# Performance work log

Hardware: AMD Instinct MI355X
Metric: run time of the kernel (lower is better)

Reference implementation:

```python
import jax, jax.numpy as jnp
import numpy as np

B, N, NONGT, D, H, PE = 128, 36, 36, 1024, 16, 64
DG = D // H  # per-head dim = 64


def setup_inputs() -> dict:
    key = jax.random.key(0)
    ks = jax.random.split(key, 10)
    s = 0.02
    return {
        "roi_feat": jax.random.normal(ks[0], (B, N, D), jnp.float32),
        "adj_matrix": jax.random.randint(ks[1], (B, N, NONGT), 0, 2, jnp.int32),
        "position_embedding": jax.random.normal(ks[2], (B, N, NONGT, PE), jnp.float32),
        "label_biases_att": jax.random.normal(ks[3], (B, N, NONGT), jnp.float32) * 0.1,
        # effective (weight-normed) linear weights
        "Wq": jax.random.normal(ks[4], (D, D), jnp.float32) * s,
        "bq": jnp.zeros((D,), jnp.float32),
        "Wk": jax.random.normal(ks[5], (D, D), jnp.float32) * s,
        "bk": jnp.zeros((D,), jnp.float32),
        "Wpos": jax.random.normal(ks[6], (H, PE), jnp.float32) * s,
        "bpos": jnp.zeros((H,), jnp.float32),
        # grouped 1x1 conv (groups=H): per-head projection feat_dim -> feat_dim/H
        "Wout": jax.random.normal(ks[7], (H, DG, D), jnp.float32) * s,
        "bout": jnp.zeros((D,), jnp.float32),
    }


def reference(roi_feat, adj_matrix, position_embedding, label_biases_att,
              Wq, bq, Wk, bk, Wpos, bpos, Wout, bout):
    b, n, d = roi_feat.shape
    nongt = adj_matrix.shape[2]
    dg = d // H
    v = roi_feat[:, :nongt, :]                                  # [B,nongt,D]
    q = (roi_feat @ Wq.T + bq).reshape(b, n, H, dg)             # [B,N,H,dg]
    k = (v @ Wk.T + bk).reshape(b, nongt, H, dg)                # [B,nongt,H,dg]
    # scaled QK^T, laid out [B,N,H,nongt] (orig: matmul then transpose(1,2))
    aff = jnp.einsum('bnhd,bmhd->bnhm', q, k) / jnp.sqrt(jnp.float32(dg))
    # position log-bias
    pos = jax.nn.relu(position_embedding.reshape(b, n * nongt, -1) @ Wpos.T + bpos)
    pos = pos.reshape(b, n, nongt, H).transpose(0, 1, 3, 2)     # [B,N,H,nongt]
    waff = aff + jnp.log(jnp.maximum(pos, jnp.float32(1e-6)))
    # adjacency mask + label bias (orig does this in [B,N,nongt,H] layout; equivalent)
    mask = adj_matrix[:, :, None, :] > 0                        # [B,N,1,nongt]
    waff = jnp.where(mask, waff, jnp.float32(-9e15)) + label_biases_att[:, :, None, :]
    att = jax.nn.softmax(waff, axis=-1)                         # [B,N,H,nongt]
    # weighted sum of full V (note: V is full feat_dim per head, not dg)
    out_t = jnp.einsum('bnhm,bmd->bnhd', att, v)                # [B,N,H,D]
    # grouped 1x1 conv: per-head D -> D/H, heads concatenated
    out = jnp.einsum('bnhd,hed->bnhe', out_t, Wout).reshape(b, n, d) + bout
    return out
```

## Files before the change

kernel.cpp:

```cpp
#include <hip/hip_runtime.h>
#include <hip/hip_bf16.h>

#define BB 128
#define NN 36
#define DD 1024
#define HH 16
#define ROWS (BB*NN)

typedef __attribute__((ext_vector_type(8))) __bf16 bf16x8;
typedef __attribute__((ext_vector_type(4))) float f32x4;
typedef __attribute__((ext_vector_type(4))) unsigned short us4;

__device__ inline unsigned short f2bf(float f) {
    __hip_bfloat16 h = __float2bfloat16(f);
    return *reinterpret_cast<unsigned short*>(&h);
}

__device__ inline void async16(const unsigned short* g, unsigned short* l) {
    __builtin_amdgcn_global_load_lds((const __attribute__((address_space(1))) unsigned int*)g,
                                     (__attribute__((address_space(3))) unsigned int*)l, 16, 0, 0);
}

__global__ __launch_bounds__(256) void prep_kernel(const float* __restrict__ roi,
                                                   const float* __restrict__ Wq,
                                                   const float* __restrict__ Wk,
                                                   const float* __restrict__ Wout,
                                                   const float* __restrict__ pe,
                                                   const float* __restrict__ Wpos,
                                                   const float* __restrict__ bpos,
                                                   const int* __restrict__ adj,
                                                   const float* __restrict__ lbl,
                                                   unsigned short* __restrict__ roi_bf,
                                                   unsigned short* __restrict__ Wcat_bf,
                                                   float* __restrict__ extra) {
    const int bid = blockIdx.x, tid = threadIdx.x;
    if (bid < 4608) {
        int i = bid * 256 + tid;
        f32x4 v = ((const f32x4*)roi)[i];
        us4 o;
        o.x = f2bf(v[0]); o.y = f2bf(v[1]); o.z = f2bf(v[2]); o.w = f2bf(v[3]);
        ((us4*)roi_bf)[i] = o;
        return;
    }
    if (bid < 7680) {
        int wb = bid - 4608;
        int sel = wb >> 10;
        const float* src = sel == 0 ? Wq : (sel == 1 ? Wk : Wout);
        int i = (wb & 1023) * 256 + tid;
        f32x4 v = ((const f32x4*)src)[i];
        us4 o;
        o.x = f2bf(v[0]); o.y = f2bf(v[1]); o.z = f2bf(v[2]); o.w = f2bf(v[3]);
        ((us4*)(Wcat_bf + (size_t)sel * DD * DD))[i] = o;
        return;
    }
    __shared__ __align__(16) float wps[HH * 64];
    __shared__ float bps[HH];
    for (int i = tid; i < HH * 64; i += 256) wps[i] = Wpos[i];
    if (tid < HH) bps[tid] = bpos[tid];
    __syncthreads();

    int idx = (bid - 7680) * 256 + tid;
    f32x4 pr[16];
    const f32x4* pv = (const f32x4*)(pe + (size_t)idx * 64);
#pragma unroll
    for (int j = 0; j < 16; j++) pr[j] = pv[j];
    int a = adj[idx];
    float add = lbl[idx] + (a > 0 ? 0.f : -9e15f);
    int b = idx / 1296, nm = idx % 1296;
    size_t obase = (size_t)b * (16 * 1296) + nm;
    for (int hh = 0; hh < 16; hh++) {
        const f32x4* wv = (const f32x4*)(wps + hh * 64);
        f32x4 acc4 = {0.f, 0.f, 0.f, 0.f};
#pragma unroll
        for (int j = 0; j < 16; j++) acc4 += pr[j] * wv[j];
        float d = acc4[0] + acc4[1] + acc4[2] + acc4[3] + bps[hh];
        d = fmaxf(d, 0.f);
        d = __logf(fmaxf(d, 1e-6f));
        extra[obase + (size_t)hh * 1296] = d + add;
    }
}

__global__ __launch_bounds__(256, 2) void fused_kernel(const unsigned short* __restrict__ A,
                                                       const unsigned short* __restrict__ Wc,
                                                       const float* __restrict__ bq,
                                                       const float* __restrict__ bk,
                                                       const float* __restrict__ extra,
                                                       const float* __restrict__ bout,
                                                       float* __restrict__ out) {
    __shared__ __align__(16) unsigned short pool[21504];
    const int tid  = threadIdx.x;
    const int wave = tid >> 6, lane = tid & 63;
    const int quad = lane >> 4, l16 = lane & 15;
    const int h  = blockIdx.x & 15;
    const int bg = blockIdx.x >> 4;
    const int row0 = bg * 144;

    unsigned short* As = pool;
    unsigned short* Bs = pool + 9216;

    const unsigned short* gsrc[11];
    unsigned short* ldst[11];
#pragma unroll
    for (int i = 0; i < 11; i++) {
        int j = wave + 4 * i;
        int c = j * 64 + lane;
        if (j < 18) {
            int row = c >> 3;
            int col = ((c & 7) ^ (row & 7)) * 8;
            gsrc[i] = A + (size_t)(row0 + row) * DD + col;
            ldst[i] = As + j * 512;
        } else {
            int cb = c - 1152;
            int row = cb >> 3;
            int sec = row >> 6;
            int wrow = sec * DD + h * 64 + (row & 63);
            int col = ((cb & 7) ^ (row & 7)) * 8;
            gsrc[i] = Wc + (size_t)wrow * DD + col;
            ldst[i] = Bs + (j - 18) * 512;
        }
    }

    f32x4 acc[9][3] = {};

#pragma unroll
    for (int k0i = 0; k0i < 16; k0i++) {
#pragma unroll
        for (int i = 0; i < 11; i++) {
            if (i < 10 || wave < 2)
                async16(gsrc[i] + k0i * 64, ldst[i]);
        }
        __syncthreads();

#pragma unroll
        for (int ks = 0; ks < 2; ks++) {
            int kch = ks * 4 + quad;
            bf16x8 bfv[3], afv[9];
#pragma unroll
            for (int ct = 0; ct < 3; ct++) {
                int rowb = wave * 48 + ct * 16 + l16;
                bfv[ct] = *(const bf16x8*)&Bs[rowb * 64 + ((kch ^ (rowb & 7)) * 8)];
            }
#pragma unroll
            for (int rt = 0; rt < 9; rt++) {
                int rowa = rt * 16 + l16;
                afv[rt] = *(const bf16x8*)&As[rowa * 64 + ((kch ^ (rowa & 7)) * 8)];
            }
#pragma unroll
            for (int rt = 0; rt < 9; rt++)
#pragma unroll
                for (int ct = 0; ct < 3; ct++)
                    acc[rt][ct] = __builtin_amdgcn_mfma_f32_16x16x32_bf16(afv[rt], bfv[ct], acc[rt][ct], 0, 0, 0);
        }
        __syncthreads();
    }

    const int bat = wave;
    const float* exb = extra + ((size_t)((bg * 4 + bat) * 16 + h)) * 1296;
    float exv[3][4][3];
#pragma unroll
    for (int mt = 0; mt < 3; mt++)
#pragma unroll
        for (int r = 0; r < 4; r++) {
            int row = mt * 16 + quad * 4 + r;
#pragma unroll
            for (int nt = 0; nt < 3; nt++) {
                int col = nt * 16 + l16;
                exv[mt][r][nt] = (row < 36 && col < 36) ? exb[row * 36 + col] : 0.f;
            }
        }
    float bo[4];
#pragma unroll
    for (int nt = 0; nt < 4; nt++) bo[nt] = bout[h * 64 + nt * 16 + l16];

    unsigned short* qL = pool;
    unsigned short* kL = pool + 10368;
#pragma unroll
    for (int ct = 0; ct < 3; ct++) {
        int g = wave * 48 + ct * 16 + l16;
        int sec = g >> 6, e = g & 63;
        if (sec < 2) {
            unsigned short* dst = (sec == 0) ? qL : kL;
            float bias = (sec == 0) ? bq[h * 64 + e] : bk[h * 64 + e];
#pragma unroll
            for (int rt = 0; rt < 9; rt++)
#pragma unroll
                for (int r = 0; r < 4; r++) {
                    int row = rt * 16 + quad * 4 + r;
                    dst[row * 72 + e] = f2bf(acc[rt][ct][r] + bias);
                }
        }
    }
    __syncthreads();

    const unsigned short* qB = qL + bat * 36 * 72;
    const unsigned short* kB = kL + bat * 36 * 72;
    int rq[3];
#pragma unroll
    for (int t = 0; t < 3; t++) { int rr = t * 16 + l16; rq[t] = rr < 36 ? rr : 35; }

    f32x4 aff[3][3] = {};
#pragma unroll
    for (int ks = 0; ks < 2; ks++) {
        bf16x8 afr[3], bfr[3];
#pragma unroll
        for (int t = 0; t < 3; t++) afr[t] = *(const bf16x8*)&qB[rq[t] * 72 + ks * 32 + quad * 8];
#pragma unroll
        for (int t = 0; t < 3; t++) bfr[t] = *(const bf16x8*)&kB[rq[t] * 72 + ks * 32 + quad * 8];
#pragma unroll
        for (int mt = 0; mt < 3; mt++)
#pragma unroll
            for (int nt = 0; nt < 3; nt++)
                aff[mt][nt] = __builtin_amdgcn_mfma_f32_16x16x32_bf16(afr[mt], bfr[nt], aff[mt][nt], 0, 0, 0);
    }
    __syncthreads();

    unsigned short* vwT   = pool;
    unsigned short* attsL = pool + 10240 + bat * 2688;
#pragma unroll
    for (int mt = 0; mt < 3; mt++) {
#pragma unroll
        for (int r = 0; r < 4; r++) {
            int row = mt * 16 + quad * 4 + r;
            float w[3];
#pragma unroll
            for (int nt = 0; nt < 3; nt++) {
                int col = nt * 16 + l16;
                bool valid = (row < 36) && (col < 36);
                w[nt] = valid ? (aff[mt][nt][r] * 0.125f + exv[mt][r][nt]) : -3.4e38f;
            }
            float mx = fmaxf(fmaxf(w[0], w[1]), w[2]);
#pragma unroll
            for (int d = 1; d < 16; d <<= 1) mx = fmaxf(mx, __shfl_xor(mx, d));
            float e0 = __expf(w[0] - mx), e1 = __expf(w[1] - mx), e2 = __expf(w[2] - mx);
            float s = e0 + e1 + e2;
#pragma unroll
            for (int d = 1; d < 16; d <<= 1) s += __shfl_xor(s, d);
            float rs = 1.0f / s;
            attsL[row * 56 + 0  + l16] = f2bf(e0 * rs);
            attsL[row * 56 + 16 + l16] = f2bf(e1 * rs);
            attsL[row * 56 + 32 + l16] = f2bf(e2 * rs);
        }
    }
#pragma unroll
    for (int ct = 0; ct < 3; ct++) {
        int g = wave * 48 + ct * 16 + l16;
        int sec = g >> 6, e = g & 63;
        if (sec == 2) {
#pragma unroll
            for (int rt = 0; rt < 9; rt++)
#pragma unroll
                for (int r = 0; r < 4; r++) {
                    int row = rt * 16 + quad * 4 + r;
                    int bb = row / 36, m = row - bb * 36;
                    vwT[bb * 2560 + e * 40 + m] = f2bf(acc[rt][ct][r]);
                }
        }
    }
    __syncthreads();

    const unsigned short* vB = vwT + bat * 2560;
    f32x4 o[3][4] = {};
    {
        bf16x8 pa[3], pb[4], zf = {};
#pragma unroll
        for (int mt = 0; mt < 3; mt++) pa[mt] = *(const bf16x8*)&attsL[(mt * 16 + l16) * 56 + quad * 8];
#pragma unroll
        for (int nt = 0; nt < 4; nt++) pb[nt] = *(const bf16x8*)&vB[(nt * 16 + l16) * 40 + quad * 8];
#pragma unroll
        for (int mt = 0; mt < 3; mt++)
#pragma unroll
            for (int nt = 0; nt < 4; nt++)
                o[mt][nt] = __builtin_amdgcn_mfma_f32_16x16x32_bf16(pa[mt], pb[nt], o[mt][nt], 0, 0, 0);
#pragma unroll
        for (int mt = 0; mt < 3; mt++)
            pa[mt] = (quad < 2) ? *(const bf16x8*)&attsL[(mt * 16 + l16) * 56 + 32 + quad * 8] : zf;
#pragma unroll
        for (int nt = 0; nt < 4; nt++)
            pb[nt] = (quad < 2) ? *(const bf16x8*)&vB[(nt * 16 + l16) * 40 + 32 + quad * 8] : zf;
#pragma unroll
        for (int mt = 0; mt < 3; mt++)
#pragma unroll
            for (int nt = 0; nt < 4; nt++)
                o[mt][nt] = __builtin_amdgcn_mfma_f32_16x16x32_bf16(pa[mt], pb[nt], o[mt][nt], 0, 0, 0);
    }

    const size_t obase = (size_t)((bg * 4 + bat) * 36) * DD + h * 64;
#pragma unroll
    for (int mt = 0; mt < 3; mt++)
#pragma unroll
        for (int r = 0; r < 4; r++) {
            int n = mt * 16 + quad * 4 + r;
            if (n < 36) {
#pragma unroll
                for (int nt = 0; nt < 4; nt++)
                    out[obase + (size_t)n * DD + nt * 16 + l16] = o[mt][nt][r] + bo[nt];
            }
        }
}

extern "C" void kernel_launch(void* const* d_in, const int* in_sizes, int n_in,
                              void* d_out, int out_size, void* d_ws, size_t ws_size,
                              hipStream_t stream) {
    const float* roi  = (const float*)d_in[0];
    const int*   adj  = (const int*)  d_in[1];
    const float* pe   = (const float*)d_in[2];
    const float* lbl  = (const float*)d_in[3];
    const float* Wq   = (const float*)d_in[4];
    const float* bq   = (const float*)d_in[5];
    const float* Wk   = (const float*)d_in[6];
    const float* bk   = (const float*)d_in[7];
    const float* Wpos = (const float*)d_in[8];
    const float* bpos = (const float*)d_in[9];
    const float* Wout = (const float*)d_in[10];
    const float* bout = (const float*)d_in[11];
    float* out = (float*)d_out;

    char* w = (char*)d_ws;
    unsigned short* roi_bf  = (unsigned short*)(w);
    unsigned short* Wcat_bf = (unsigned short*)(w + 9437184);
    float*          extra   = (float*)(w + 15728640);

    prep_kernel<<<8328, 256, 0, stream>>>(roi, Wq, Wk, Wout, pe, Wpos, bpos, adj, lbl,
                                          roi_bf, Wcat_bf, extra);
    fused_kernel<<<32 * 16, 256, 0, stream>>>(roi_bf, Wcat_bf, bq, bk, extra, bout, out);
}
```

Baseline: 170.7 us.

## Replace async global-to-LDS loads with register-staged prefetch of next K tile

Switches the GEMM tile staging from direct global_load_lds intrinsics to loading the next K-slice into registers while the current slice is computed, then writing registers to LDS. This is meant to overlap global memory latency with MFMA work, where before each step waited on its own loads. It costs 11 extra vector registers per thread and an explicit LDS store pass, which could hurt occupancy under the 2-blocks launch bound. It also clamps an out-of-range B row index.

```diff
diff --git a/kernel.cpp b/kernel.cpp
--- a/kernel.cpp
+++ b/kernel.cpp
@@ -14,11 +14,6 @@
 __device__ inline unsigned short f2bf(float f) {
     __hip_bfloat16 h = __float2bfloat16(f);
     return *reinterpret_cast<unsigned short*>(&h);
-}
-
-__device__ inline void async16(const unsigned short* g, unsigned short* l) {
-    __builtin_amdgcn_global_load_lds((const __attribute__((address_space(1))) unsigned int*)g,
-                                     (__attribute__((address_space(3))) unsigned int*)l, 16, 0, 0);
 }
 
 __global__ __launch_bounds__(256) void prep_kernel(const float* __restrict__ roi,
@@ -98,8 +93,8 @@
     unsigned short* As = pool;
     unsigned short* Bs = pool + 9216;
 
-    const unsigned short* gsrc[11];
-    unsigned short* ldst[11];
+    const f32x4* gsrc[11];
+    f32x4* ldst[11];
 #pragma unroll
     for (int i = 0; i < 11; i++) {
         int j = wave + 4 * i;
@@ -107,29 +102,42 @@
         if (j < 18) {
             int row = c >> 3;
             int col = ((c & 7) ^ (row & 7)) * 8;
-            gsrc[i] = A + (size_t)(row0 + row) * DD + col;
-            ldst[i] = As + j * 512;
+            gsrc[i] = (const f32x4*)(A + (size_t)(row0 + row) * DD + col);
+            ldst[i] = (f32x4*)(As + j * 512 + lane * 8);
         } else {
             int cb = c - 1152;
             int row = cb >> 3;
+            if (row > 191) row = 191;
             int sec = row >> 6;
             int wrow = sec * DD + h * 64 + (row & 63);
             int col = ((cb & 7) ^ (row & 7)) * 8;
-            gsrc[i] = Wc + (size_t)wrow * DD + col;
-            ldst[i] = Bs + (j - 18) * 512;
+            gsrc[i] = (const f32x4*)(Wc + (size_t)wrow * DD + col);
+            ldst[i] = (f32x4*)(Bs + (j - 18) * 512 + lane * 8);
         }
     }
 
     f32x4 acc[9][3] = {};
+    f32x4 rbuf[11];
+
+#pragma unroll
+    for (int i = 0; i < 11; i++)
+        if (i < 10 || wave < 2)
+            rbuf[i] = gsrc[i][0];
 
 #pragma unroll
     for (int k0i = 0; k0i < 16; k0i++) {
 #pragma unroll
-        for (int i = 0; i < 11; i++) {
+        for (int i = 0; i < 11; i++)
             if (i < 10 || wave < 2)
-                async16(gsrc[i] + k0i * 64, ldst[i]);
-        }
+                *ldst[i] = rbuf[i];
         __syncthreads();
+
+        if (k0i < 15) {
+#pragma unroll
+            for (int i = 0; i < 11; i++)
+                if (i < 10 || wave < 2)
+                    rbuf[i] = gsrc[i][(k0i + 1) * 8];
+        }
 
 #pragma unroll
         for (int ks = 0; ks < 2; ks++) {
```

New measurement: 173.7 us. About the same (+1.8%).
